# Kernel optimization log

Measured on AMD Instinct MI355X. Metric: run time of the kernel, lower is better.

## Reference

```python
import jax, jax.numpy as jnp
import numpy as np

N, E, F, H, G, C = 50000, 800000, 128, 128, 500, 10
L = 3  # num_conv_layers
EPS = 1e-5


def batch_norm(x, g, b):
    # training-mode BatchNorm1d: biased variance, eps=1e-5
    mu = jnp.mean(x, axis=0)
    var = jnp.var(x, axis=0)
    return (x - mu) * jax.lax.rsqrt(var + EPS) * g + b


def gcn_conv(x, W, bias, src, dst, n):
    # x' = D^{-1/2} (A + I) D^{-1/2} (x W) + bias, edge weights = 1
    xw = x @ W
    loop = jnp.arange(n)
    s = jnp.concatenate([src, loop])  # sources incl. self-loops
    d = jnp.concatenate([dst, loop])  # targets incl. self-loops
    w = jnp.ones(s.shape[0], x.dtype)
    deg = jax.ops.segment_sum(w, s, num_segments=n)
    dinv = jnp.where(deg > 0, jax.lax.rsqrt(deg), 0.0)
    norm = dinv[s] * w * dinv[d]
    msg = xw[s] * norm[:, None]  # gather + scale
    out = jax.ops.segment_sum(msg, d, num_segments=n)  # scatter-add
    return out + bias


def setup_inputs() -> dict:
    key = jax.random.key(0)
    ks = jax.random.split(key, 16)
    x = jax.random.normal(ks[0], (N, F), dtype=jnp.float32)
    edge_index = jax.random.randint(ks[1], (2, E), 0, N, dtype=jnp.int64)
    batch = jnp.sort(jax.random.randint(ks[2], (N,), 0, G, dtype=jnp.int64))
    sF = 1.0 / np.sqrt(F)
    sH = 1.0 / np.sqrt(H)
    return {
        "x": x,
        "edge_index": edge_index,
        "batch": batch,
        "bn_feat_g": jnp.ones((F,), jnp.float32),
        "bn_feat_b": jnp.full((F,), 1e-4, jnp.float32),
        "W_feat": jax.random.normal(ks[3], (F, H), jnp.float32) * sF,
        "bns_conv_g": jnp.ones((L, H), jnp.float32),
        "bns_conv_b": jnp.full((L, H), 1e-4, jnp.float32),
        "W_conv": jax.random.normal(ks[4], (L, H, H), jnp.float32) * sH,
        "b_conv": jnp.zeros((L, H), jnp.float32),
        "bn_fc_g": jnp.ones((H,), jnp.float32),
        "bn_fc_b": jnp.full((H,), 1e-4, jnp.float32),
        "W_lin": jax.random.normal(ks[5], (H, H), jnp.float32) * sH,
        "b_lin": jnp.zeros((H,), jnp.float32),
        "bn_hid_g": jnp.ones((H,), jnp.float32),
        "bn_hid_b": jnp.full((H,), 1e-4, jnp.float32),
        "W_cls": jax.random.normal(ks[6], (H, C), jnp.float32) * sH,
        "b_cls": jnp.zeros((C,), jnp.float32),
    }


def reference(x, edge_index, batch, bn_feat_g, bn_feat_b, W_feat,
              bns_conv_g, bns_conv_b, W_conv, b_conv,
              bn_fc_g, bn_fc_b, W_lin, b_lin,
              bn_hid_g, bn_hid_b, W_cls, b_cls):
    src, dst = edge_index[0], edge_index[1]
    h = batch_norm(x, bn_feat_g, bn_feat_b)
    h = jax.nn.relu(h @ W_feat)  # gfn conv: linear only, no bias/propagation
    for i in range(L):
        h = batch_norm(h, bns_conv_g[i], bns_conv_b[i])
        h = jax.nn.relu(gcn_conv(h, W_conv[i], b_conv[i], src, dst, N))
    h = jax.ops.segment_sum(h, batch, num_segments=G)  # global_add_pool
    h = batch_norm(h, bn_fc_g, bn_fc_b)
    h = jax.nn.relu(h @ W_lin + b_lin)
    h = batch_norm(h, bn_hid_g, bn_hid_b)
    logits = h @ W_cls + b_cls
    return jax.nn.log_softmax(logits, axis=-1)
```

## Files before the change

### kernel.cpp

```cpp
#include <hip/hip_runtime.h>

#define NF 128
#define EPS 1e-5f
#define KELL 64
#define HB 64
#define HRANGE 32768
#define BCAP 5120

typedef unsigned short ushort_t;
typedef unsigned int uint_t;

using bf16x8 = __attribute__((ext_vector_type(8))) short;
using f32x4  = __attribute__((ext_vector_type(4))) float;

static __device__ inline ushort_t f2bf(float f) {
    uint_t u = __float_as_uint(f);
    return (ushort_t)((u + 0x7fffu + ((u >> 16) & 1u)) >> 16);
}


__launch_bounds__(1024)
__global__ void k_prep(const int* __restrict__ ei, uint_t* __restrict__ gcnt,
                       uint_t* __restrict__ bedge, uint_t* __restrict__ hpart,
                       const float* __restrict__ W0, const float* __restrict__ W123,
                       ushort_t* __restrict__ Wp, int E) {
    __shared__ union {
        struct { uint_t cnt[256]; uint_t cur[256]; uint_t base[256]; } bk;
        uint_t h2[HRANGE / 2];
    } sh;
    const int blk = blockIdx.x;
    const int t = threadIdx.x;

    if (blk < 256) {
        if (t < 256) { sh.bk.cnt[t] = 0; sh.bk.cur[t] = 0; }
        __syncthreads();
        const int chunk = (E + 255) / 256;
        const int e0 = blk * chunk;
        const int e1 = min(e0 + chunk, E);
        for (int e = e0 + t; e < e1; e += 1024)
            atomicAdd(&sh.bk.cnt[ei[E + e] >> 8], 1);
        __syncthreads();
        if (t < 256) {
            uint_t c = sh.bk.cnt[t];
            sh.bk.base[t] = c ? atomicAdd(&gcnt[t], c) : 0u;
        }
        __syncthreads();
        for (int e = e0 + t; e < e1; e += 1024) {
            int s = ei[e], d = ei[E + e];
            int b = d >> 8;
            uint_t pos = sh.bk.base[b] + atomicAdd(&sh.bk.cur[b], 1);
            if (pos < BCAP)
                bedge[((size_t)b << 12) + ((size_t)b << 10) + pos] =
                    ((uint_t)(d & 255) << 16) | (uint_t)s;
        }
    } else if (blk < 320) {
        const int b = blk - 256;
#pragma unroll
        for (int p = 0; p < 2; ++p) {
            int base = p * HRANGE;
            for (int w = t; w < HRANGE / 2; w += 1024) sh.h2[w] = 0;
            __syncthreads();
            for (int e = b * 1024 + t; e < E; e += HB * 1024) {
                unsigned u = (unsigned)(ei[e] - base);
                if (u < HRANGE)
                    atomicAdd(&sh.h2[u >> 1], 1u << ((u & 1) << 4));
            }
            __syncthreads();
            uint_t* dst = hpart + ((size_t)(p * HB + b) << 14);
            for (int w = t; w < HRANGE / 2; w += 1024) dst[w] = sh.h2[w];
            __syncthreads();
        }
    } else {
#pragma unroll
        for (int kk = 0; kk < 4; ++kk) {
            int gidx = (blk - 320) * 4096 + kk * 1024 + t;
            int mat = gidx >> 11, idx = gidx & 2047;
            const float* W = (mat == 0) ? W0 : (W123 + (size_t)(mat - 1) * NF * NF);
            int lane = idx & 63, ct = (idx >> 6) & 7, kc = idx >> 9;
            int m = lane & 15, q = lane >> 4;
            ushort_t o[8];
#pragma unroll
            for (int j = 0; j < 8; ++j)
                o[j] = f2bf(W[(kc * 32 + q * 8 + j) * NF + ct * 16 + m]);
            *(uint4*)&Wp[(size_t)gidx * 8] = *(uint4*)o;
        }
    }
}

__launch_bounds__(256)
__global__ void k_build(const uint_t* __restrict__ gcnt, const uint_t* __restrict__ bedge,
                        const uint_t* __restrict__ hpart, int* __restrict__ ucnt,
                        float* __restrict__ dinv, ushort_t* __restrict__ colx,
                        ushort_t* __restrict__ BbSent, int n) {
    __shared__ ushort_t ell[256][KELL];
    __shared__ uint_t lcnt[256];
    const int b = blockIdx.x, t = threadIdx.x;
    lcnt[t] = 0;
    __syncthreads();
    const int nb = min((int)gcnt[b], BCAP);
    const int node0 = b << 8;
    const uint_t* bsrc = bedge + ((size_t)b << 12) + ((size_t)b << 10);
    for (int e = t; e < nb; e += 256) {
        uint_t pk = bsrc[e];
        int dl = (pk >> 16) & 255;
        uint_t pos = atomicAdd(&lcnt[dl], 1);
        if (pos < KELL - 1) ell[dl][pos] = (ushort_t)(pk & 0xffffu);
    }
    __syncthreads();
    const int i = node0 + t;
    if (i < n) {
        int w = min((int)lcnt[t], KELL - 1);
        ell[t][w] = (ushort_t)i;
        int len = (w + 16) & ~15;
        for (int q = w + 1; q < len; ++q) ell[t][q] = (ushort_t)n;
        ucnt[i] = w;
        int p = i >> 15;
        int u = i & (HRANGE - 1);
        int wd = u >> 1, sh = (u & 1) << 4;
        const uint_t* basep = hpart + ((size_t)(p * HB) << 14) + wd;
        uint_t sum = 0;
#pragma unroll 8
        for (int bb = 0; bb < HB; ++bb) sum += basep[(size_t)bb << 14];
        sum = (sum >> sh) & 0xffffu;
        dinv[i] = rsqrtf((float)sum + 1.0f);
    }
    __syncthreads();
    int nrow = min(n - node0, 256);
    if (nrow > 0) {
        const uint4* src = (const uint4*)&ell[0][0];
        uint4* dst = (uint4*)&colx[(size_t)node0 * KELL];
        int lim = nrow * (KELL * 2 / 16);
        for (int wds = t; wds < lim; wds += 256) dst[wds] = src[wds];
    }
    if (b == 0 && t < 64)
        ((uint_t*)BbSent)[t] = 0;
}


__global__ void bn_stats(const float* __restrict__ h, float* __restrict__ stats, int n) {
    int j = threadIdx.x & 127;
    int half = threadIdx.x >> 7;
    float s = 0.f, q = 0.f;
    for (int r = blockIdx.x * 2 + half; r < n; r += gridDim.x * 2) {
        float v = h[r * NF + j];
        s += v;
        q += v * v;
    }
    __shared__ float ls[256], lq[256];
    ls[threadIdx.x] = s; lq[threadIdx.x] = q;
    __syncthreads();
    if (threadIdx.x < 128) {
        atomicAdd(&stats[j], ls[threadIdx.x] + ls[threadIdx.x + 128]);
        atomicAdd(&stats[NF + j], lq[threadIdx.x] + lq[threadIdx.x + 128]);
    }
}


#define HSTRIDE 136

__launch_bounds__(512)
__global__ void gemm_mfma(const float* __restrict__ Hh, const ushort_t* __restrict__ Wp,
                          const float* __restrict__ stats, const float* __restrict__ gW,
                          const float* __restrict__ bB, float inv_n,
                          const float* __restrict__ bias, const float* __restrict__ rowscale,
                          float* __restrict__ out, ushort_t* __restrict__ outb,
                          float* __restrict__ statsOut,
                          int nrows, int relu, int obf) {
    __shared__ union {
        ushort_t hs[64 * HSTRIDE];
        float    ob[32][132];
        ushort_t obu[64][136];
    } shu;
    __shared__ float acs[256];
    __shared__ float cs[128], cq[128];
    const int tid = threadIdx.x;
    const int rb = blockIdx.x * 64;

    if (tid < 128) {
        float mean = stats[tid] * inv_n;
        float var = stats[NF + tid] * inv_n - mean * mean;
        float rstd = rsqrtf(var + EPS);
        float a = gW[tid] * rstd;
        acs[tid] = a;
        acs[NF + tid] = bB[tid] - mean * a;
        cs[tid] = 0.f; cq[tid] = 0.f;
    }
    __syncthreads();
    const float4* ac4 = (const float4*)acs;

#pragma unroll
    for (int p = 0; p < 4; ++p) {
        int idx = p * 512 + tid;
        int r = idx >> 5, k4 = idx & 31;
        int gr = rb + r;
        float4 v = (gr < nrows) ? *(const float4*)&Hh[(size_t)gr * NF + k4 * 4]
                                : make_float4(0.f, 0.f, 0.f, 0.f);
        float4 a4 = ac4[k4], c4 = ac4[32 + k4];
        ushort_t o[4];
        o[0] = f2bf(fmaf(v.x, a4.x, c4.x));
        o[1] = f2bf(fmaf(v.y, a4.y, c4.y));
        o[2] = f2bf(fmaf(v.z, a4.z, c4.z));
        o[3] = f2bf(fmaf(v.w, a4.w, c4.w));
        *(uint2*)&shu.hs[r * HSTRIDE + k4 * 4] = *(uint2*)o;
    }
    __syncthreads();

    const int wave = tid >> 6, lane = tid & 63;
    const int wr = wave & 3;
    const int wc = wave >> 2;
    const int m = lane & 15, q = lane >> 4;
    const ushort_t* arow = &shu.hs[(wr * 16 + m) * HSTRIDE];

    f32x4 acc[4];
#pragma unroll
    for (int ct = 0; ct < 4; ++ct) acc[ct] = (f32x4){0.f, 0.f, 0.f, 0.f};

#pragma unroll
    for (int kc = 0; kc < 4; ++kc) {
        bf16x8 af = *(const bf16x8*)&arow[kc * 32 + q * 8];
        const ushort_t* wp = Wp + kc * 4096 + (wc * 4) * 512 + lane * 8;
#pragma unroll
        for (int ct = 0; ct < 4; ++ct) {
            bf16x8 bfr = *(const bf16x8*)&wp[ct * 512];
            acc[ct] = __builtin_amdgcn_mfma_f32_16x16x32_bf16(af, bfr, acc[ct], 0, 0, 0);
        }
    }

    int grows[4]; float rsv[4]; bool gv[4];
#pragma unroll
    for (int r = 0; r < 4; ++r) {
        grows[r] = rb + wr * 16 + q * 4 + r;
        gv[r] = grows[r] < nrows;
        rsv[r] = (obf && rowscale && gv[r]) ? rowscale[grows[r]] : 1.0f;
    }

    if (statsOut) {
#pragma unroll
        for (int ct = 0; ct < 4; ++ct) {
            int col = (wc * 4 + ct) * 16 + m;
            float bcol = bias ? bias[col] : 0.f;
            float s = 0.f, qq = 0.f;
#pragma unroll
            for (int r = 0; r < 4; ++r) {
                if (gv[r]) {
                    float v = acc[ct][r] + bcol;
                    if (relu) v = fmaxf(v, 0.f);
                    s += v; qq += v * v;
                }
            }
            atomicAdd(&cs[col], s); atomicAdd(&cq[col], qq);
        }
    }

    __syncthreads();

    if (obf) {
#pragma unroll
        for (int ct = 0; ct < 4; ++ct) {
            int col = (wc * 4 + ct) * 16 + m;
            float bcol = bias ? bias[col] : 0.f;
#pragma unroll
            for (int r = 0; r < 4; ++r) {
                int row = wr * 16 + q * 4 + r;
                float v = acc[ct][r] + bcol;
                if (relu) v = fmaxf(v, 0.f);
                shu.obu[row][col] = f2bf(v * rsv[r]);
            }
        }
        __syncthreads();
#pragma unroll
        for (int i = 0; i < 2; ++i) {
            int idx = i * 512 + tid;
            int r = idx >> 4, c8 = idx & 15;
            int grow = rb + r;
            if (grow < nrows)
                *(uint4*)&outb[(size_t)grow * NF + c8 * 8] =
                    *(const uint4*)&shu.obu[r][c8 * 8];
        }
    } else {
#pragma unroll
        for (int h = 0; h < 2; ++h) {
            if ((wr >> 1) == h) {
#pragma unroll
                for (int ct = 0; ct < 4; ++ct) {
                    int col = (wc * 4 + ct) * 16 + m;
                    float bcol = bias ? bias[col] : 0.f;
#pragma unroll
                    for (int r = 0; r < 4; ++r) {
                        int row = (wr & 1) * 16 + q * 4 + r;
                        float v = acc[ct][r] + bcol;
                        if (relu) v = fmaxf(v, 0.f);
                        shu.ob[row][col] = v;
                    }
                }
            }
            __syncthreads();
#pragma unroll
            for (int i = 0; i < 2; ++i) {
                int idx = i * 512 + tid;
                int r = idx >> 5, c4 = idx & 31;
                int grow = rb + h * 32 + r;
                if (grow < nrows)
                    *(float4*)&out[(size_t)grow * NF + c4 * 4] =
                        *(const float4*)&shu.ob[r][c4 * 4];
            }
            __syncthreads();
        }
    }

    if (statsOut) {
        if (tid < 128) {
            atomicAdd(&statsOut[tid], cs[tid]);
            atomicAdd(&statsOut[NF + tid], cq[tid]);
        }
    }
}


__launch_bounds__(256)
__global__ void gemm_bn(const float* __restrict__ Hh, const float* __restrict__ W,
                        const float* __restrict__ stats, const float* __restrict__ gW,
                        const float* __restrict__ bB, float inv_n,
                        const float* __restrict__ bias,
                        float* __restrict__ out, float* __restrict__ statsOut,
                        int nrows, int relu) {
    __shared__ float hsb[64][133];
    __shared__ float acs[256];
    __shared__ float cs[128], cq[128];
    const int tid = threadIdx.x;
    const int tx = tid & 15;
    const int ty = tid >> 4;
    const int rb = blockIdx.x * 64;

    if (tid < 128) {
        float mean = stats[tid] * inv_n;
        float var = stats[NF + tid] * inv_n - mean * mean;
        float rstd = rsqrtf(var + EPS);
        float a = gW[tid] * rstd;
        acs[tid] = a;
        acs[NF + tid] = bB[tid] - mean * a;
        cs[tid] = 0.f; cq[tid] = 0.f;
    }
    __syncthreads();

#pragma unroll 8
    for (int p = 0; p < 32; ++p) {
        int idx = p * 256 + tid;
        int r = idx >> 7, k = idx & 127;
        int gr = rb + r;
        float v = (gr < nrows) ? Hh[(size_t)gr * NF + k] : 0.f;
        hsb[r][k] = fmaf(v, acs[k], acs[NF + k]);
    }
    __syncthreads();

    float acc[4][8];
#pragma unroll
    for (int i = 0; i < 4; ++i)
#pragma unroll
        for (int j = 0; j < 8; ++j) acc[i][j] = 0.f;

    const int c0 = tx * 4, c1 = 64 + tx * 4;
#pragma unroll 4
    for (int k = 0; k < 128; ++k) {
        const float4 b0 = *(const float4*)&W[k * NF + c0];
        const float4 b1 = *(const float4*)&W[k * NF + c1];
#pragma unroll
        for (int i = 0; i < 4; ++i) {
            float a = hsb[ty * 4 + i][k];
            acc[i][0] = fmaf(a, b0.x, acc[i][0]);
            acc[i][1] = fmaf(a, b0.y, acc[i][1]);
            acc[i][2] = fmaf(a, b0.z, acc[i][2]);
            acc[i][3] = fmaf(a, b0.w, acc[i][3]);
            acc[i][4] = fmaf(a, b1.x, acc[i][4]);
            acc[i][5] = fmaf(a, b1.y, acc[i][5]);
            acc[i][6] = fmaf(a, b1.z, acc[i][6]);
            acc[i][7] = fmaf(a, b1.w, acc[i][7]);
        }
    }

    float scol[8], qcol[8];
#pragma unroll
    for (int j = 0; j < 8; ++j) { scol[j] = 0.f; qcol[j] = 0.f; }
#pragma unroll
    for (int i = 0; i < 4; ++i) {
        int gr = rb + ty * 4 + i;
        if (gr < nrows) {
            float o[8];
#pragma unroll
            for (int j = 0; j < 8; ++j) {
                int c = (j < 4) ? (c0 + j) : (c1 + j - 4);
                float v = acc[i][j] + (bias ? bias[c] : 0.f);
                o[j] = relu ? fmaxf(v, 0.f) : v;
                scol[j] += o[j]; qcol[j] += o[j] * o[j];
            }
            *(float4*)&out[(size_t)gr * NF + c0] = make_float4(o[0], o[1], o[2], o[3]);
            *(float4*)&out[(size_t)gr * NF + c1] = make_float4(o[4], o[5], o[6], o[7]);
        }
    }
    if (statsOut) {
#pragma unroll
        for (int j = 0; j < 8; ++j) {
            int c = (j < 4) ? (c0 + j) : (c1 + j - 4);
            atomicAdd(&cs[c], scol[j]);
            atomicAdd(&cq[c], qcol[j]);
        }
        __syncthreads();
        if (tid < 128) {
            atomicAdd(&statsOut[tid], cs[tid]);
            atomicAdd(&statsOut[NF + tid], cq[tid]);
        }
    }
}


#define CVT2(u, a, b) { a = __uint_as_float((u) << 16); b = __uint_as_float((u) & 0xffff0000u); }
#define ACC8(q) { float p0, p1, p2, p3, p4, p5, p6, p7;                          \
    CVT2(q.x, p0, p1) CVT2(q.y, p2, p3) CVT2(q.z, p4, p5) CVT2(q.w, p6, p7)      \
    acc[0] += p0; acc[1] += p1; acc[2] += p2; acc[3] += p3;                      \
    acc[4] += p4; acc[5] += p5; acc[6] += p6; acc[7] += p7; }

__launch_bounds__(256)
__global__ void k_aggregate_bf(const ushort_t* __restrict__ xwb, const int* __restrict__ ucnt,
                               const ushort_t* __restrict__ colx, const float* __restrict__ dinv,
                               const float* __restrict__ bias, float* __restrict__ out, int n) {
    int node = blockIdx.x * 16 + (threadIdx.x >> 4);
    int lane = threadIdx.x & 15;
    if (node >= n) return;
    const uint4* __restrict__ xq = (const uint4*)xwb;
    float acc[8];
#pragma unroll
    for (int j = 0; j < 8; ++j) acc[j] = 0.f;
    int dc = min(ucnt[node], KELL - 1);
    int len = (dc + 16) & ~15;
    int e0 = node * KELL;
    for (int e = e0; e < e0 + len; e += 16) {
        uint4 ia = *(const uint4*)&colx[e];
        uint4 ib = *(const uint4*)&colx[e + 8];
        int i0 = ia.x & 0xffff, i1 = ia.x >> 16;
        int i2 = ia.y & 0xffff, i3 = ia.y >> 16;
        int i4 = ia.z & 0xffff, i5 = ia.z >> 16;
        int i6 = ia.w & 0xffff, i7 = ia.w >> 16;
        int i8 = ib.x & 0xffff, i9 = ib.x >> 16;
        int iA = ib.y & 0xffff, iB = ib.y >> 16;
        int iC = ib.z & 0xffff, iD = ib.z >> 16;
        int iE = ib.w & 0xffff, iF = ib.w >> 16;
        uint4 q0 = xq[(size_t)i0 * 16 + lane];
        uint4 q1 = xq[(size_t)i1 * 16 + lane];
        uint4 q2 = xq[(size_t)i2 * 16 + lane];
        uint4 q3 = xq[(size_t)i3 * 16 + lane];
        uint4 q4 = xq[(size_t)i4 * 16 + lane];
        uint4 q5 = xq[(size_t)i5 * 16 + lane];
        uint4 q6 = xq[(size_t)i6 * 16 + lane];
        uint4 q7 = xq[(size_t)i7 * 16 + lane];
        uint4 q8 = xq[(size_t)i8 * 16 + lane];
        uint4 q9 = xq[(size_t)i9 * 16 + lane];
        uint4 qA = xq[(size_t)iA * 16 + lane];
        uint4 qB = xq[(size_t)iB * 16 + lane];
        uint4 qC = xq[(size_t)iC * 16 + lane];
        uint4 qD = xq[(size_t)iD * 16 + lane];
        uint4 qE = xq[(size_t)iE * 16 + lane];
        uint4 qF = xq[(size_t)iF * 16 + lane];
        ACC8(q0) ACC8(q1) ACC8(q2) ACC8(q3)
        ACC8(q4) ACC8(q5) ACC8(q6) ACC8(q7)
        ACC8(q8) ACC8(q9) ACC8(qA) ACC8(qB)
        ACC8(qC) ACC8(qD) ACC8(qE) ACC8(qF)
    }
    float di = dinv[node];
    float4 b0 = *(const float4*)&bias[lane * 8];
    float4 b1 = *(const float4*)&bias[lane * 8 + 4];
    float4 o0, o1;
    o0.x = fmaxf(fmaf(di, acc[0], b0.x), 0.f);
    o0.y = fmaxf(fmaf(di, acc[1], b0.y), 0.f);
    o0.z = fmaxf(fmaf(di, acc[2], b0.z), 0.f);
    o0.w = fmaxf(fmaf(di, acc[3], b0.w), 0.f);
    o1.x = fmaxf(fmaf(di, acc[4], b1.x), 0.f);
    o1.y = fmaxf(fmaf(di, acc[5], b1.y), 0.f);
    o1.z = fmaxf(fmaf(di, acc[6], b1.z), 0.f);
    o1.w = fmaxf(fmaf(di, acc[7], b1.w), 0.f);
    *(float4*)&out[(size_t)node * NF + lane * 8] = o0;
    *(float4*)&out[(size_t)node * NF + lane * 8 + 4] = o1;
}


__global__ void k_pool(const float* __restrict__ h, const int* __restrict__ batch,
                       float* __restrict__ pooled, float* __restrict__ stats, int n) {
    int g = blockIdx.x;
    int t = threadIdx.x;
    int lo = 0, hi = n;
    while (lo < hi) { int m = (lo + hi) >> 1; if (batch[m] < g) lo = m + 1; else hi = m; }
    int start = lo;
    lo = start; hi = n;
    while (lo < hi) { int m = (lo + hi) >> 1; if (batch[m] < g + 1) lo = m + 1; else hi = m; }
    int end = lo;
    float a0 = 0.f, a1 = 0.f, a2 = 0.f, a3 = 0.f;
    int r = start;
    for (; r + 4 <= end; r += 4) {
        a0 += h[(size_t)r * NF + t];
        a1 += h[(size_t)(r + 1) * NF + t];
        a2 += h[(size_t)(r + 2) * NF + t];
        a3 += h[(size_t)(r + 3) * NF + t];
    }
    for (; r < end; ++r) a0 += h[(size_t)r * NF + t];
    float val = (a0 + a1) + (a2 + a3);
    pooled[g * NF + t] = val;
    atomicAdd(&stats[t], val);
    atomicAdd(&stats[NF + t], val * val);
}


__global__ void k_cls(const float* __restrict__ h, const float* __restrict__ stats,
                      const float* __restrict__ gW, const float* __restrict__ bB,
                      float inv_n, const float* __restrict__ Wc,
                      const float* __restrict__ bc, float* __restrict__ out, int C_) {
    __shared__ float hr[128];
    __shared__ float lg[16];
    __shared__ float lse_s;
    int r = blockIdx.x, t = threadIdx.x;
#pragma unroll
    for (int half = 0; half < 2; ++half) {
        int j = t + half * 64;
        float mean = stats[j] * inv_n;
        float var = stats[NF + j] * inv_n - mean * mean;
        float rstd = rsqrtf(var + EPS);
        float a = gW[j] * rstd;
        float c = bB[j] - mean * a;
        hr[j] = fmaf(h[r * NF + j], a, c);
    }
    __syncthreads();
    if (t < C_) {
        float s = bc[t];
        for (int k = 0; k < 128; ++k) s = fmaf(hr[k], Wc[k * C_ + t], s);
        lg[t] = s;
    }
    __syncthreads();
    if (t == 0) {
        float m = -1e30f;
        for (int c = 0; c < C_; ++c) m = fmaxf(m, lg[c]);
        float se = 0.f;
        for (int c = 0; c < C_; ++c) se += expf(lg[c] - m);
        lse_s = m + logf(se);
    }
    __syncthreads();
    if (t < C_) out[r * C_ + t] = lg[t] - lse_s;
}


extern "C" void kernel_launch(void* const* d_in, const int* in_sizes, int n_in,
                              void* d_out, int out_size, void* d_ws, size_t ws_size,
                              hipStream_t stream) {
    const float* x          = (const float*)d_in[0];
    const int*   ei         = (const int*)d_in[1];
    const int*   batch      = (const int*)d_in[2];
    const float* bn_feat_g  = (const float*)d_in[3];
    const float* bn_feat_b  = (const float*)d_in[4];
    const float* W_feat     = (const float*)d_in[5];
    const float* bns_conv_g = (const float*)d_in[6];
    const float* bns_conv_b = (const float*)d_in[7];
    const float* W_conv     = (const float*)d_in[8];
    const float* b_conv     = (const float*)d_in[9];
    const float* bn_fc_g    = (const float*)d_in[10];
    const float* bn_fc_b    = (const float*)d_in[11];
    const float* W_lin      = (const float*)d_in[12];
    const float* b_lin      = (const float*)d_in[13];
    const float* bn_hid_g   = (const float*)d_in[14];
    const float* bn_hid_b   = (const float*)d_in[15];
    const float* W_cls      = (const float*)d_in[16];
    const float* b_cls      = (const float*)d_in[17];
    float* outp = (float*)d_out;

    const int N_ = in_sizes[2];
    const int E_ = in_sizes[1] / 2;
    const int C_ = 10;
    const int G_ = out_size / C_;
    const int NBUCK = (N_ + 255) >> 8;

    char* wsp = (char*)d_ws;
    auto alloc = [&](size_t bytes) {
        void* p = (void*)wsp;
        wsp += (bytes + 255) & ~(size_t)255;
        return p;
    };
    uint_t*   gcnt   = (uint_t*)alloc(256 * 4);
    float*    statsA = (float*)alloc(6 * 256 * 4);
    float*    A      = (float*)alloc((size_t)N_ * NF * 4);
    ushort_t* Bb     = (ushort_t*)alloc((size_t)(N_ + 1) * NF * 2);
    float*    dinv   = (float*)alloc((size_t)N_ * 4);
    int*      ucnt   = (int*)alloc((size_t)N_ * 4);
    uint_t*   bedge  = (uint_t*)alloc((size_t)256 * BCAP * 4);
    ushort_t* colx   = (ushort_t*)alloc((size_t)N_ * KELL * 2);
    uint_t*   hpart  = (uint_t*)alloc((size_t)2 * HB * (HRANGE / 2) * 4);
    ushort_t* Wp     = (ushort_t*)alloc((size_t)4 * NF * NF * 2);
    float*    pooled = (float*)alloc((size_t)G_ * NF * 4);
    float*    y2     = (float*)alloc((size_t)G_ * NF * 4);

    float* st_x  = statsA;
    float* st_f  = statsA + 256;
    float* st_a1 = statsA + 512;
    float* st_a2 = statsA + 768;
    float* st_pl = statsA + 1024;
    float* st_y2 = statsA + 1280;

    int nb_g = (N_ + 63) / 64;

    hipMemsetAsync(gcnt, 0, 1024 + 6 * 256 * 4, stream);

    k_prep<<<322, 1024, 0, stream>>>(ei, gcnt, bedge, hpart, W_feat, W_conv, Wp, E_);
    k_build<<<NBUCK, 256, 0, stream>>>(gcnt, bedge, hpart, ucnt, dinv, colx,
                                       Bb + (size_t)N_ * NF, N_);

    bn_stats<<<512, 256, 0, stream>>>(x, st_x, N_);
    gemm_mfma<<<nb_g, 512, 0, stream>>>(x, Wp, st_x, bn_feat_g, bn_feat_b, 1.0f / N_,
                                        nullptr, nullptr, A, nullptr, st_f, N_, 1, 0);

    float* st_in[3] = {st_f, st_a1, st_a2};
    float* st_out[3] = {st_a1, st_a2, nullptr};
    for (int l = 0; l < 3; ++l) {
        gemm_mfma<<<nb_g, 512, 0, stream>>>(A, Wp + (size_t)(l + 1) * NF * NF,
                                            st_in[l], bns_conv_g + l * NF, bns_conv_b + l * NF,
                                            1.0f / N_, nullptr, dinv, nullptr, Bb, nullptr,
                                            N_, 0, 1);
        k_aggregate_bf<<<(N_ + 15) / 16, 256, 0, stream>>>(Bb, ucnt, colx, dinv,
                                                           b_conv + l * NF, A, N_);
        if (st_out[l])
            bn_stats<<<512, 256, 0, stream>>>(A, st_out[l], N_);
    }

    k_pool<<<G_, 128, 0, stream>>>(A, batch, pooled, st_pl, N_);

    gemm_bn<<<(G_ + 63) / 64, 256, 0, stream>>>(pooled, W_lin, st_pl, bn_fc_g, bn_fc_b,
                                                1.0f / G_, b_lin, y2, st_y2, G_, 1);

    k_cls<<<G_, 64, 0, stream>>>(y2, st_y2, bn_hid_g, bn_hid_b, 1.0f / G_,
                                 W_cls, b_cls, outp, C_);
}
```

Baseline: 428.1 us.

## Store intermediate activations in bf16 and fold input BN stats into prep kernel

Intermediate activations between layers are now written and read as bf16 instead of fp32. This covers the first linear layer output and the first two aggregation outputs, which feed the next GEMM and the BN statistics. The aim is to halve memory traffic for those tensors. Separately, the input BN statistics are computed by extra blocks appended to the prep kernel, which removes a launch and overlaps that work with the graph preprocessing. The cost is bf16 rounding of activations before the statistics are taken, which slightly changes numerics, though the GEMM already rounded its inputs to bf16.

After: 411.7 us. -3.8%, faster.

```diff
diff --git a/kernel.cpp b/kernel.cpp
--- a/kernel.cpp
+++ b/kernel.cpp
@@ -6,6 +6,7 @@
 #define HB 64
 #define HRANGE 32768
 #define BCAP 5120
+#define SB 512
 
 typedef unsigned short ushort_t;
 typedef unsigned int uint_t;
@@ -23,10 +24,12 @@
 __global__ void k_prep(const int* __restrict__ ei, uint_t* __restrict__ gcnt,
                        uint_t* __restrict__ bedge, uint_t* __restrict__ hpart,
                        const float* __restrict__ W0, const float* __restrict__ W123,
-                       ushort_t* __restrict__ Wp, int E) {
+                       ushort_t* __restrict__ Wp, const float* __restrict__ x,
+                       float* __restrict__ stx, int E, int n) {
     __shared__ union {
         struct { uint_t cnt[256]; uint_t cur[256]; uint_t base[256]; } bk;
         uint_t h2[HRANGE / 2];
+        struct { float ls[1024]; float lq[1024]; } st;
     } sh;
     const int blk = blockIdx.x;
     const int t = threadIdx.x;
@@ -70,7 +73,7 @@
             for (int w = t; w < HRANGE / 2; w += 1024) dst[w] = sh.h2[w];
             __syncthreads();
         }
-    } else {
+    } else if (blk < 322) {
 #pragma unroll
         for (int kk = 0; kk < 4; ++kk) {
             int gidx = (blk - 320) * 4096 + kk * 1024 + t;
@@ -83,6 +86,27 @@
             for (int j = 0; j < 8; ++j)
                 o[j] = f2bf(W[(kc * 32 + q * 8 + j) * NF + ct * 16 + m]);
             *(uint4*)&Wp[(size_t)gidx * 8] = *(uint4*)o;
+        }
+    } else {
+        const int b = blk - 322;
+        const int j = t & 127;
+        const int row8 = t >> 7;
+        float s = 0.f, q = 0.f;
+        for (int r = b * 8 + row8; r < n; r += SB * 8) {
+            float v = x[(size_t)r * NF + j];
+            s += v; q += v * v;
+        }
+        sh.st.ls[t] = s; sh.st.lq[t] = q;
+        __syncthreads();
+        if (t < 128) {
+            float ss = 0.f, qq = 0.f;
+#pragma unroll
+            for (int k = 0; k < 8; ++k) {
+                ss += sh.st.ls[t + k * 128];
+                qq += sh.st.lq[t + k * 128];
+            }
+            atomicAdd(&stx[t], ss);
+            atomicAdd(&stx[NF + t], qq);
         }
     }
 }
@@ -137,12 +161,12 @@
 }
 
 
-__global__ void bn_stats(const float* __restrict__ h, float* __restrict__ stats, int n) {
+__global__ void bn_stats_bf(const ushort_t* __restrict__ h, float* __restrict__ stats, int n) {
     int j = threadIdx.x & 127;
     int half = threadIdx.x >> 7;
     float s = 0.f, q = 0.f;
     for (int r = blockIdx.x * 2 + half; r < n; r += gridDim.x * 2) {
-        float v = h[r * NF + j];
+        float v = __uint_as_float((uint_t)h[(size_t)r * NF + j] << 16);
         s += v;
         q += v * v;
     }
@@ -159,7 +183,7 @@
 #define HSTRIDE 136
 
 __launch_bounds__(512)
-__global__ void gemm_mfma(const float* __restrict__ Hh, const ushort_t* __restrict__ Wp,
+__global__ void gemm_mfma(const void* __restrict__ In, int inbf, const ushort_t* __restrict__ Wp,
                           const float* __restrict__ stats, const float* __restrict__ gW,
                           const float* __restrict__ bB, float inv_n,
                           const float* __restrict__ bias, const float* __restrict__ rowscale,
@@ -193,8 +217,18 @@
         int idx = p * 512 + tid;
         int r = idx >> 5, k4 = idx & 31;
         int gr = rb + r;
-        float4 v = (gr < nrows) ? *(const float4*)&Hh[(size_t)gr * NF + k4 * 4]
-                                : make_float4(0.f, 0.f, 0.f, 0.f);
+        float4 v = make_float4(0.f, 0.f, 0.f, 0.f);
+        if (gr < nrows) {
+            if (inbf) {
+                uint2 u = *(const uint2*)((const ushort_t*)In + (size_t)gr * NF + k4 * 4);
+                v.x = __uint_as_float(u.x << 16);
+                v.y = __uint_as_float(u.x & 0xffff0000u);
+                v.z = __uint_as_float(u.y << 16);
+                v.w = __uint_as_float(u.y & 0xffff0000u);
+            } else {
+                v = *(const float4*)((const float*)In + (size_t)gr * NF + k4 * 4);
+            }
+        }
         float4 a4 = ac4[k4], c4 = ac4[32 + k4];
         ushort_t o[4];
         o[0] = f2bf(fmaf(v.x, a4.x, c4.x));
@@ -422,7 +456,8 @@
 __launch_bounds__(256)
 __global__ void k_aggregate_bf(const ushort_t* __restrict__ xwb, const int* __restrict__ ucnt,
                                const ushort_t* __restrict__ colx, const float* __restrict__ dinv,
-                               const float* __restrict__ bias, float* __restrict__ out, int n) {
+                               const float* __restrict__ bias, float* __restrict__ out,
+                               ushort_t* __restrict__ outb, int n) {
     int node = blockIdx.x * 16 + (threadIdx.x >> 4);
     int lane = threadIdx.x & 15;
     if (node >= n) return;
@@ -477,8 +512,15 @@
     o1.y = fmaxf(fmaf(di, acc[5], b1.y), 0.f);
     o1.z = fmaxf(fmaf(di, acc[6], b1.z), 0.f);
     o1.w = fmaxf(fmaf(di, acc[7], b1.w), 0.f);
-    *(float4*)&out[(size_t)node * NF + lane * 8] = o0;
-    *(float4*)&out[(size_t)node * NF + lane * 8 + 4] = o1;
+    if (outb) {
+        ushort_t ob[8];
+        ob[0] = f2bf(o0.x); ob[1] = f2bf(o0.y); ob[2] = f2bf(o0.z); ob[3] = f2bf(o0.w);
+        ob[4] = f2bf(o1.x); ob[5] = f2bf(o1.y); ob[6] = f2bf(o1.z); ob[7] = f2bf(o1.w);
+        *(uint4*)&outb[(size_t)node * NF + lane * 8] = *(uint4*)ob;
+    } else {
+        *(float4*)&out[(size_t)node * NF + lane * 8] = o0;
+        *(float4*)&out[(size_t)node * NF + lane * 8 + 4] = o1;
+    }
 }
 
 
@@ -583,6 +625,7 @@
     uint_t*   gcnt   = (uint_t*)alloc(256 * 4);
     float*    statsA = (float*)alloc(6 * 256 * 4);
     float*    A      = (float*)alloc((size_t)N_ * NF * 4);
+    ushort_t* Ab     = (ushort_t*)alloc((size_t)N_ * NF * 2);
     ushort_t* Bb     = (ushort_t*)alloc((size_t)(N_ + 1) * NF * 2);
     float*    dinv   = (float*)alloc((size_t)N_ * 4);
     int*      ucnt   = (int*)alloc((size_t)N_ * 4);
@@ -604,25 +647,29 @@
 
     hipMemsetAsync(gcnt, 0, 1024 + 6 * 256 * 4, stream);
 
-    k_prep<<<322, 1024, 0, stream>>>(ei, gcnt, bedge, hpart, W_feat, W_conv, Wp, E_);
+    k_prep<<<322 + SB, 1024, 0, stream>>>(ei, gcnt, bedge, hpart, W_feat, W_conv, Wp,
+                                          x, st_x, E_, N_);
     k_build<<<NBUCK, 256, 0, stream>>>(gcnt, bedge, hpart, ucnt, dinv, colx,
                                        Bb + (size_t)N_ * NF, N_);
 
-    bn_stats<<<512, 256, 0, stream>>>(x, st_x, N_);
-    gemm_mfma<<<nb_g, 512, 0, stream>>>(x, Wp, st_x, bn_feat_g, bn_feat_b, 1.0f / N_,
-                                        nullptr, nullptr, A, nullptr, st_f, N_, 1, 0);
+    gemm_mfma<<<nb_g, 512, 0, stream>>>(x, 0, Wp, st_x, bn_feat_g, bn_feat_b, 1.0f / N_,
+                                        nullptr, nullptr, nullptr, Ab, st_f, N_, 1, 1);
 
     float* st_in[3] = {st_f, st_a1, st_a2};
     float* st_out[3] = {st_a1, st_a2, nullptr};
     for (int l = 0; l < 3; ++l) {
-        gemm_mfma<<<nb_g, 512, 0, stream>>>(A, Wp + (size_t)(l + 1) * NF * NF,
+        gemm_mfma<<<nb_g, 512, 0, stream>>>(Ab, 1, Wp + (size_t)(l + 1) * NF * NF,
                                             st_in[l], bns_conv_g + l * NF, bns_conv_b + l * NF,
                                             1.0f / N_, nullptr, dinv, nullptr, Bb, nullptr,
                                             N_, 0, 1);
-        k_aggregate_bf<<<(N_ + 15) / 16, 256, 0, stream>>>(Bb, ucnt, colx, dinv,
-                                                           b_conv + l * NF, A, N_);
-        if (st_out[l])
-            bn_stats<<<512, 256, 0, stream>>>(A, st_out[l], N_);
+        if (l < 2) {
+            k_aggregate_bf<<<(N_ + 15) / 16, 256, 0, stream>>>(Bb, ucnt, colx, dinv,
+                                                               b_conv + l * NF, nullptr, Ab, N_);
+            bn_stats_bf<<<512, 256, 0, stream>>>(Ab, st_out[l], N_);
+        } else {
+            k_aggregate_bf<<<(N_ + 15) / 16, 256, 0, stream>>>(Bb, ucnt, colx, dinv,
+                                                               b_conv + l * NF, A, nullptr, N_);
+        }
     }
 
     k_pool<<<G_, 128, 0, stream>>>(A, batch, pooled, st_pl, N_);
```
